# Kernel optimization log

Measured on AMD Instinct MI355X. Metric: run time of the kernel, lower is better.

Reference implementation:

```python
import jax, jax.numpy as jnp
import numpy as np

D = 1024      # n_embd
F = 1024      # moe_inter_dim (ffn_hidden_size)
E = 8         # moe_num_experts
K = 2         # moe_top_k
B, T = 2, 2048


def setup_inputs() -> dict:
    key = jax.random.key(0)
    ks = jax.random.split(key, 7)
    std = 0.02
    x = jax.random.normal(ks[0], (B, T, D), dtype=jnp.float32)
    router_w = jax.random.normal(ks[1], (D, E), dtype=jnp.float32) * std
    w1 = jax.random.normal(ks[2], (E, D, F), dtype=jnp.float32) * std  # expert up proj
    w2 = jax.random.normal(ks[3], (E, F, D), dtype=jnp.float32) * std  # expert down proj
    shared_gate_up = jax.random.normal(ks[4], (D, 2 * F), dtype=jnp.float32) * std
    shared_down = jax.random.normal(ks[5], (F, D), dtype=jnp.float32) * std
    shared_gate_w = jax.random.normal(ks[6], (D, 1), dtype=jnp.float32) * std
    return {"x": x, "router_w": router_w, "w1": w1, "w2": w2,
            "shared_gate_up": shared_gate_up, "shared_down": shared_down,
            "shared_gate_w": shared_gate_w}


def _moe_forward(x, router_w, w1, w2, shared_gate_up, shared_down, shared_gate_w):
    b, t, d = x.shape
    xf = x.reshape(-1, d)                                   # [N, D]
    n = xf.shape[0]

    # --- router: softmax over experts, top-k scores used directly as combine weights ---
    logits = xf @ router_w                                  # [N, E]
    probs = jax.nn.softmax(logits, axis=-1)
    topw, topi = jax.lax.top_k(probs, K)                    # [N, K]
    combine = jnp.zeros((n, E), dtype=probs.dtype).at[
        jnp.arange(n)[:, None], topi].add(topw)             # [N, E] sparse combine weights

    # --- expert MLP: h = silu(x @ w1_e) @ w2_e, combined with routing weights ---
    h = jax.nn.silu(jnp.einsum('nd,edf->nef', xf, w1))      # [N, E, F]
    ye = jnp.einsum('nef,efd->ned', h, w2)                  # [N, E, D]
    routed = jnp.einsum('ne,ned->nd', combine, ye)          # [N, D]

    # --- shared expert SwiGLU, gated by sigmoid(x @ shared_gate_w) ---
    gu = xf @ shared_gate_up                                # [N, 2F]
    gate, up = gu[:, :F], gu[:, F:]
    shared = (jax.nn.silu(gate) * up) @ shared_down         # [N, D]
    shared = jax.nn.sigmoid(xf @ shared_gate_w) * shared

    return (routed + shared).reshape(b, t, d)


def reference(x, router_w, w1, w2, shared_gate_up, shared_down, shared_gate_w):
    return _moe_forward(x, router_w, w1, w2, shared_gate_up, shared_down, shared_gate_w)
```

## Files before the change

kernel.cpp:

```cpp
#include <hip/hip_runtime.h>
#include <math.h>

typedef __bf16 bf16_t;
typedef __bf16 bf16x8 __attribute__((ext_vector_type(8)));
typedef __bf16 bf16x4 __attribute__((ext_vector_type(4)));
typedef float f32x4 __attribute__((ext_vector_type(4)));

#define N_TOK 4096
#define DMODEL 1024
#define FFN 1024
#define NEXP 8
#define HIST_BLK 16

#define BM 128
#define BN 128
#define BK 32
#define LDK 32

__device__ __forceinline__ void gload16(const bf16_t* g, bf16_t* l) {
  __builtin_amdgcn_global_load_lds((const __attribute__((address_space(1))) void*)g,
                                   (__attribute__((address_space(3))) void*)l, 16, 0, 0);
}

__global__ void transpose_all_kernel(const float* __restrict__ w1, const float* __restrict__ w2,
                                     const float* __restrict__ sgu, const float* __restrict__ sdw,
                                     bf16_t* __restrict__ w1t, bf16_t* __restrict__ w2t,
                                     bf16_t* __restrict__ sgut, bf16_t* __restrict__ sdt) {
  __shared__ float tile[32][33];
  const int z = blockIdx.z;
  const float* in;
  bf16_t* out;
  int C = 1024;
  bool remap = false;
  if (z < 8) {
    in = w1 + (size_t)z * 1048576; out = w1t + (size_t)z * 1048576;
  } else if (z < 16) {
    in = w2 + (size_t)(z - 8) * 1048576; out = w2t + (size_t)(z - 8) * 1048576;
  } else if (z == 16) {
    in = sgu; out = sgut; C = 2048; remap = true;
  } else {
    in = sdw; out = sdt;
  }
  const int R = 1024;
  const int c0 = blockIdx.x * 32, r0 = blockIdx.y * 32;
  if (c0 >= C) return;
  const int tx = threadIdx.x, ty = threadIdx.y;
#pragma unroll
  for (int i = 0; i < 32; i += 8)
    tile[ty + i][tx] = in[(size_t)(r0 + ty + i) * C + (c0 + tx)];
  __syncthreads();
#pragma unroll
  for (int i = 0; i < 32; i += 8) {
    int c = c0 + ty + i;
    int oc = remap ? ((c < FFN) ? 2 * c : 2 * (c - FFN) + 1) : c;
    out[(size_t)oc * R + (r0 + tx)] = (bf16_t)tile[tx][ty + i];
  }
}

__global__ void router_kernel(const float* __restrict__ x, const float* __restrict__ rw,
                              const float* __restrict__ gw, bf16_t* __restrict__ xb,
                              int* __restrict__ topi, float* __restrict__ topw,
                              float* __restrict__ sig) {
  const int t = blockIdx.x;
  const int lane = threadIdx.x;
  const float* xr = x + (size_t)t * DMODEL;
  bf16_t* xbr = xb + (size_t)t * DMODEL;
  float acc[NEXP] = {0.f, 0.f, 0.f, 0.f, 0.f, 0.f, 0.f, 0.f};
  float accg = 0.f;
#pragma unroll
  for (int i = 0; i < 4; i++) {
    const int d = i * 256 + lane * 4;
    float4 xv = *reinterpret_cast<const float4*>(xr + d);
    bf16x4 o;
    o[0] = (bf16_t)xv.x; o[1] = (bf16_t)xv.y; o[2] = (bf16_t)xv.z; o[3] = (bf16_t)xv.w;
    *reinterpret_cast<bf16x4*>(xbr + d) = o;
    const float xs[4] = {xv.x, xv.y, xv.z, xv.w};
#pragma unroll
    for (int j = 0; j < 4; j++) {
      const float4* r = reinterpret_cast<const float4*>(rw + (size_t)(d + j) * NEXP);
      float4 r0 = r[0], r1 = r[1];
      float xj = xs[j];
      acc[0] += xj * r0.x; acc[1] += xj * r0.y; acc[2] += xj * r0.z; acc[3] += xj * r0.w;
      acc[4] += xj * r1.x; acc[5] += xj * r1.y; acc[6] += xj * r1.z; acc[7] += xj * r1.w;
      accg += xj * gw[d + j];
    }
  }
#pragma unroll
  for (int e = 0; e < NEXP; e++)
    for (int s = 32; s > 0; s >>= 1) acc[e] += __shfl_down(acc[e], s, 64);
  for (int s = 32; s > 0; s >>= 1) accg += __shfl_down(accg, s, 64);
  if (lane == 0) {
    float mx = acc[0];
#pragma unroll
    for (int e = 1; e < NEXP; e++) mx = fmaxf(mx, acc[e]);
    float p[NEXP], sum = 0.f;
#pragma unroll
    for (int e = 0; e < NEXP; e++) { p[e] = __expf(acc[e] - mx); sum += p[e]; }
    int i1 = 0;
#pragma unroll
    for (int e = 1; e < NEXP; e++) if (acc[e] > acc[i1]) i1 = e;
    int i2 = (i1 == 0) ? 1 : 0;
#pragma unroll
    for (int e = 0; e < NEXP; e++) if (e != i1 && acc[e] > acc[i2]) i2 = e;
    float inv = 1.f / sum;
    topi[2 * t] = i1;     topw[2 * t] = p[i1] * inv;
    topi[2 * t + 1] = i2; topw[2 * t + 1] = p[i2] * inv;
    sig[t] = 1.f / (1.f + __expf(-accg));
  }
}

__global__ void hist_kernel(const int* __restrict__ topi, int* __restrict__ block_counts) {
  __shared__ int h[NEXP];
  const int tid = threadIdx.x;
  if (tid < NEXP) h[tid] = 0;
  __syncthreads();
  const int t = blockIdx.x * 256 + tid;
  atomicAdd(&h[topi[2 * t]], 1);
  atomicAdd(&h[topi[2 * t + 1]], 1);
  __syncthreads();
  if (tid < NEXP) block_counts[blockIdx.x * NEXP + tid] = h[tid];
}

__global__ void gather_kernel(const int* __restrict__ topi, const float* __restrict__ topw,
                              const int* __restrict__ block_counts, int* __restrict__ slot_tok,
                              float* __restrict__ slot_w, int* __restrict__ slot_of,
                              int* __restrict__ offsets, int* __restrict__ counts) {
  __shared__ int cur[NEXP];
  const int tid = threadIdx.x;
  if (tid < NEXP) {
    int off = 0;
    for (int f = 0; f < tid; f++)
      for (int b = 0; b < HIST_BLK; b++) off += block_counts[b * NEXP + f];
    int bb = off;
    for (int b = 0; b < (int)blockIdx.x; b++) bb += block_counts[b * NEXP + tid];
    cur[tid] = bb;
    if (blockIdx.x == 0) {
      offsets[tid] = off;
      int tot = 0;
      for (int b = 0; b < HIST_BLK; b++) tot += block_counts[b * NEXP + tid];
      counts[tid] = tot;
    }
  }
  __syncthreads();
  const int t = blockIdx.x * 256 + tid;
#pragma unroll
  for (int j = 0; j < 2; j++) {
    int e = topi[2 * t + j];
    int s = atomicAdd(&cur[e], 1);
    slot_tok[s] = t;
    slot_w[s] = topw[2 * t + j];
    slot_of[2 * t + j] = s;
  }
}

__global__ void combine_kernel(const bf16_t* __restrict__ Y, const int* __restrict__ slot_of,
                               float* __restrict__ out) {
  int i = blockIdx.x * blockDim.x + threadIdx.x;
  int t = i >> 7;
  int d = (i & 127) << 3;
  int s0 = slot_of[2 * t], s1 = slot_of[2 * t + 1];
  bf16x8 a = *reinterpret_cast<const bf16x8*>(Y + (size_t)s0 * DMODEL + d);
  bf16x8 b = *reinterpret_cast<const bf16x8*>(Y + (size_t)s1 * DMODEL + d);
  float* o = out + (size_t)t * DMODEL + d;
  float4 o0 = *reinterpret_cast<float4*>(o);
  float4 o1 = *reinterpret_cast<float4*>(o + 4);
  o0.x += (float)a[0] + (float)b[0]; o0.y += (float)a[1] + (float)b[1];
  o0.z += (float)a[2] + (float)b[2]; o0.w += (float)a[3] + (float)b[3];
  o1.x += (float)a[4] + (float)b[4]; o1.y += (float)a[5] + (float)b[5];
  o1.z += (float)a[6] + (float)b[6]; o1.w += (float)a[7] + (float)b[7];
  *reinterpret_cast<float4*>(o) = o0;
  *reinterpret_cast<float4*>(o + 4) = o1;
}

template <int MODE>
__global__ __launch_bounds__(256) void gemm_kernel(
    const bf16_t* __restrict__ A, const bf16_t* __restrict__ B, void* __restrict__ Cout,
    int N, const int* __restrict__ offsets, const int* __restrict__ counts,
    const int* __restrict__ slot_tok, const float* __restrict__ slot_w,
    const float* __restrict__ sig) {
  __shared__ bf16_t lds_a[BM * LDK];
  __shared__ bf16_t lds_b[BN * LDK];

  int bx_l, by_l, e_l;
  {
    const int bx = blockIdx.x, by = blockIdx.y, bz = blockIdx.z;
    if (MODE == 0) {
      const int f = by * 16 + bx;
      const int k = f & 7, s = f >> 3;
      by_l = k * 4 + (s & 3); bx_l = s >> 2; e_l = 0;
    } else if (MODE == 3) {
      const int f = by * 8 + bx;
      const int k = f & 7, s = f >> 3;
      by_l = k * 4 + (s & 3); bx_l = s >> 2; e_l = 0;
    } else {
      const int f = (bz * 32 + by) * 8 + bx;
      e_l = f & 7;
      const int s = f >> 3;
      by_l = s & 31; bx_l = s >> 5;
    }
  }

  const int e = e_l;
  int m0, mEnd;
  const bf16_t* Bp = B;
  if (MODE == 1 || MODE == 2) {
    const int off = offsets[e], cnt = counts[e];
    m0 = off + by_l * BM;
    mEnd = off + cnt;
    if (m0 >= mEnd) return;
    Bp += (size_t)e * FFN * DMODEL;
  } else {
    m0 = by_l * BM;
    mEnd = N_TOK;
  }
  const int n0 = bx_l * BN;

  const int tid = threadIdx.x;
  const int lane = tid & 63;
  const int wave = tid >> 6;
  const int wm = (wave >> 1) * 64;
  const int wn = (wave & 1) * 64;
  const int qd = lane >> 4;
  const int lm = lane & 15;

  const int srow = wave * 16 + (lane >> 2);
  const int chunk = (lane & 3) ^ ((lane >> 3) & 3);
  const bf16_t* pa[2];
  const bf16_t* pb[2];
#pragma unroll
  for (int h = 0; h < 2; h++) {
    int s = m0 + srow + h * 64;
    int sc = (s < mEnd) ? s : (mEnd - 1);
    int g;
    if (MODE == 1) g = slot_tok[sc];
    else if (MODE == 2) g = sc;
    else g = s;
    pa[h] = A + (size_t)g * 1024 + chunk * 8;
    pb[h] = Bp + (size_t)(n0 + srow + h * 64) * 1024 + chunk * 8;
  }
  bf16_t* la[2] = {&lds_a[(wave * 16) * LDK], &lds_a[(64 + wave * 16) * LDK]};
  bf16_t* lb[2] = {&lds_b[(wave * 16) * LDK], &lds_b[(64 + wave * 16) * LDK]};

  f32x4 acc[4][4] = {};

  const int rkey = (lm >> 1) & 3;

  for (int k0 = 0; k0 < 1024; k0 += BK) {
    __syncthreads();
#pragma unroll
    for (int h = 0; h < 2; h++) {
      gload16(pa[h] + k0, la[h]);
      gload16(pb[h] + k0, lb[h]);
    }
    __syncthreads();
    bf16x8 af[4], bfr[4];
#pragma unroll
    for (int i = 0; i < 4; i++)
      af[i] = *reinterpret_cast<const bf16x8*>(
          &lds_a[(wm + i * 16 + lm) * LDK + ((qd ^ rkey) * 8)]);
#pragma unroll
    for (int j = 0; j < 4; j++)
      bfr[j] = *reinterpret_cast<const bf16x8*>(
          &lds_b[(wn + j * 16 + lm) * LDK + ((qd ^ rkey) * 8)]);
#pragma unroll
    for (int i = 0; i < 4; i++)
#pragma unroll
      for (int j = 0; j < 4; j++)
        acc[i][j] = __builtin_amdgcn_mfma_f32_16x16x32_bf16(af[i], bfr[j], acc[i][j], 0, 0, 0);
  }

#pragma unroll
  for (int i = 0; i < 4; i++) {
#pragma unroll
    for (int r = 0; r < 4; r++) {
      const int gm = m0 + wm + i * 16 + qd * 4 + r;
      const bool mOk = (MODE == 0 || MODE == 3) || (gm < mEnd);
      const float wgt = (MODE == 2 && mOk) ? slot_w[gm] : 0.f;
#pragma unroll
      for (int j = 0; j < 4; j++) {
        const int col = n0 + wn + j * 16 + lm;
        float v = acc[i][j][r];
        if (MODE == 0) {
          float u = __shfl_xor(v, 1, 64);
          if ((lane & 1) == 0) {
            float sv = v / (1.f + __expf(-v)) * u;
            ((bf16_t*)Cout)[(size_t)gm * FFN + (col >> 1)] = (bf16_t)sv;
          }
        } else if (MODE == 1) {
          if (mOk) ((bf16_t*)Cout)[(size_t)gm * FFN + col] = (bf16_t)(v / (1.f + __expf(-v)));
        } else if (MODE == 2) {
          if (mOk) ((bf16_t*)Cout)[(size_t)gm * DMODEL + col] = (bf16_t)(wgt * v);
        } else {
          ((float*)Cout)[(size_t)gm * DMODEL + col] = sig[gm] * v;
        }
      }
    }
  }
}

extern "C" void kernel_launch(void* const* d_in, const int* in_sizes, int n_in, void* d_out,
                              int out_size, void* d_ws, size_t ws_size, hipStream_t stream) {
  const float* x = (const float*)d_in[0];
  const float* rw = (const float*)d_in[1];
  const float* w1 = (const float*)d_in[2];
  const float* w2 = (const float*)d_in[3];
  const float* sgu = (const float*)d_in[4];
  const float* sdw = (const float*)d_in[5];
  const float* gw = (const float*)d_in[6];
  float* out = (float*)d_out;

  char* ws = (char*)d_ws;
  size_t off = 0;
  auto alloc = [&](size_t bytes) -> void* {
    void* p = ws + off;
    off += (bytes + 255) & ~(size_t)255;
    return p;
  };
  bf16_t* xb = (bf16_t*)alloc((size_t)N_TOK * DMODEL * 2);
  bf16_t* w1t = (bf16_t*)alloc((size_t)NEXP * DMODEL * FFN * 2);
  bf16_t* w2t = (bf16_t*)alloc((size_t)NEXP * DMODEL * FFN * 2);
  bf16_t* sgut = (bf16_t*)alloc((size_t)2 * FFN * DMODEL * 2);
  bf16_t* sdt = (bf16_t*)alloc((size_t)DMODEL * FFN * 2);
  bf16_t* S = (bf16_t*)alloc((size_t)N_TOK * FFN * 2);
  bf16_t* H = (bf16_t*)alloc((size_t)N_TOK * 2 * FFN * 2);
  bf16_t* Y = (bf16_t*)alloc((size_t)N_TOK * 2 * DMODEL * 2);
  int* topi = (int*)alloc(N_TOK * 2 * 4);
  float* topw = (float*)alloc(N_TOK * 2 * 4);
  float* sig = (float*)alloc(N_TOK * 4);
  int* slot_tok = (int*)alloc(N_TOK * 2 * 4);
  float* slot_w = (float*)alloc(N_TOK * 2 * 4);
  int* slot_of = (int*)alloc(N_TOK * 2 * 4);
  int* block_counts = (int*)alloc(HIST_BLK * NEXP * 4);
  int* counts = (int*)alloc(NEXP * 4);
  int* offsets = (int*)alloc(NEXP * 4);

  transpose_all_kernel<<<dim3(64, 32, 18), dim3(32, 8), 0, stream>>>(w1, w2, sgu, sdw, w1t, w2t,
                                                                     sgut, sdt);
  router_kernel<<<N_TOK, 64, 0, stream>>>(x, rw, gw, xb, topi, topw, sig);
  hist_kernel<<<HIST_BLK, 256, 0, stream>>>(topi, block_counts);
  gather_kernel<<<HIST_BLK, 256, 0, stream>>>(topi, topw, block_counts, slot_tok, slot_w,
                                              slot_of, offsets, counts);

  gemm_kernel<0><<<dim3(2 * FFN / BN, N_TOK / BM, 1), 256, 0, stream>>>(
      xb, sgut, S, 2 * FFN, nullptr, nullptr, nullptr, nullptr, nullptr);
  gemm_kernel<1><<<dim3(FFN / BN, N_TOK / BM, NEXP), 256, 0, stream>>>(
      xb, w1t, H, FFN, offsets, counts, slot_tok, nullptr, nullptr);
  gemm_kernel<2><<<dim3(DMODEL / BN, N_TOK / BM, NEXP), 256, 0, stream>>>(
      H, w2t, Y, DMODEL, offsets, counts, slot_tok, slot_w, nullptr);
  gemm_kernel<3><<<dim3(DMODEL / BN, N_TOK / BM, 1), 256, 0, stream>>>(
      S, sdt, out, DMODEL, nullptr, nullptr, nullptr, nullptr, sig);
  combine_kernel<<<N_TOK * DMODEL / 8 / 256, 256, 0, stream>>>(Y, slot_of, out);
}
```

Baseline: 279.1 us.

## Double-buffer LDS tiles in grouped GEMM to overlap loads with MFMA

Splits the shared-memory A/B tiles into two ping-pong buffers. The next K-slice is prefetched with global_load_lds into one buffer while MFMAs consume the other. The main loop is manually unrolled by two, with a single barrier per stage. This aims to hide global-to-LDS latency that was previously exposed between the two barriers. It doubles LDS use per block, which may lower occupancy.

```diff
diff --git a/kernel.cpp b/kernel.cpp
--- a/kernel.cpp
+++ b/kernel.cpp
@@ -178,8 +178,10 @@
     int N, const int* __restrict__ offsets, const int* __restrict__ counts,
     const int* __restrict__ slot_tok, const float* __restrict__ slot_w,
     const float* __restrict__ sig) {
-  __shared__ bf16_t lds_a[BM * LDK];
-  __shared__ bf16_t lds_b[BN * LDK];
+  __shared__ bf16_t lds_a0[BM * LDK];
+  __shared__ bf16_t lds_b0[BN * LDK];
+  __shared__ bf16_t lds_a1[BM * LDK];
+  __shared__ bf16_t lds_b1[BN * LDK];
 
   int bx_l, by_l, e_l;
   {
@@ -238,36 +240,46 @@
     pa[h] = A + (size_t)g * 1024 + chunk * 8;
     pb[h] = Bp + (size_t)(n0 + srow + h * 64) * 1024 + chunk * 8;
   }
-  bf16_t* la[2] = {&lds_a[(wave * 16) * LDK], &lds_a[(64 + wave * 16) * LDK]};
-  bf16_t* lb[2] = {&lds_b[(wave * 16) * LDK], &lds_b[(64 + wave * 16) * LDK]};
 
   f32x4 acc[4][4] = {};
-
   const int rkey = (lm >> 1) & 3;
 
-  for (int k0 = 0; k0 < 1024; k0 += BK) {
+#define STAGE(AB, BB, T)                                       \
+  do {                                                         \
+    const int k0s = (T) * BK;                                  \
+    gload16(pa[0] + k0s, &AB[(wave * 16) * LDK]);              \
+    gload16(pa[1] + k0s, &AB[(64 + wave * 16) * LDK]);         \
+    gload16(pb[0] + k0s, &BB[(wave * 16) * LDK]);              \
+    gload16(pb[1] + k0s, &BB[(64 + wave * 16) * LDK]);         \
+  } while (0)
+
+#define COMPUTE(AB, BB)                                                      \
+  do {                                                                       \
+    bf16x8 af[4], bfr[4];                                                    \
+    _Pragma("unroll") for (int i = 0; i < 4; i++)                            \
+        af[i] = *reinterpret_cast<const bf16x8*>(                            \
+            &AB[(wm + i * 16 + lm) * LDK + ((qd ^ rkey) * 8)]);              \
+    _Pragma("unroll") for (int j = 0; j < 4; j++)                            \
+        bfr[j] = *reinterpret_cast<const bf16x8*>(                           \
+            &BB[(wn + j * 16 + lm) * LDK + ((qd ^ rkey) * 8)]);              \
+    _Pragma("unroll") for (int i = 0; i < 4; i++)                            \
+        _Pragma("unroll") for (int j = 0; j < 4; j++)                        \
+            acc[i][j] = __builtin_amdgcn_mfma_f32_16x16x32_bf16(             \
+                af[i], bfr[j], acc[i][j], 0, 0, 0);                          \
+  } while (0)
+
+  STAGE(lds_a0, lds_b0, 0);
+  __syncthreads();
+  for (int t = 0; t < 32; t += 2) {
+    STAGE(lds_a1, lds_b1, t + 1);
+    COMPUTE(lds_a0, lds_b0);
     __syncthreads();
-#pragma unroll
-    for (int h = 0; h < 2; h++) {
-      gload16(pa[h] + k0, la[h]);
-      gload16(pb[h] + k0, lb[h]);
-    }
+    if (t + 2 < 32) STAGE(lds_a0, lds_b0, t + 2);
+    COMPUTE(lds_a1, lds_b1);
     __syncthreads();
-    bf16x8 af[4], bfr[4];
-#pragma unroll
-    for (int i = 0; i < 4; i++)
-      af[i] = *reinterpret_cast<const bf16x8*>(
-          &lds_a[(wm + i * 16 + lm) * LDK + ((qd ^ rkey) * 8)]);
-#pragma unroll
-    for (int j = 0; j < 4; j++)
-      bfr[j] = *reinterpret_cast<const bf16x8*>(
-          &lds_b[(wn + j * 16 + lm) * LDK + ((qd ^ rkey) * 8)]);
-#pragma unroll
-    for (int i = 0; i < 4; i++)
-#pragma unroll
-      for (int j = 0; j < 4; j++)
-        acc[i][j] = __builtin_amdgcn_mfma_f32_16x16x32_bf16(af[i], bfr[j], acc[i][j], 0, 0, 0);
-  }
+  }
+#undef COMPUTE
+#undef STAGE
 
 #pragma unroll
   for (int i = 0; i < 4; i++) {
```

After: 277.9 us (median of 2 runs). No clear change (-0.4%).
